# Optimization experiments

Hardware: AMD Instinct MI355X
Metric: run time of the kernel (lower is better)

Reference implementation:

```python
import jax, jax.numpy as jnp
import numpy as np

N_NODES = 100000
N_EDGES = 3200000
F_IN = 128
HIDDEN = 16
OUT_DIM = 16
NUM_GRAPHS = 64


def setup_inputs() -> dict:
    key = jax.random.key(0)
    ks = jax.random.split(key, 9)
    x = jax.random.normal(ks[0], (N_NODES, F_IN), dtype=jnp.float32)
    edge_index = jax.random.randint(ks[1], (2, N_EDGES), 0, N_NODES, dtype=jnp.int32)
    batch = jnp.sort(jax.random.randint(ks[2], (N_NODES,), 0, NUM_GRAPHS, dtype=jnp.int32))
    W1 = jax.random.normal(ks[3], (F_IN, HIDDEN), dtype=jnp.float32) * (1.0 / np.sqrt(F_IN))
    b1 = jnp.zeros((HIDDEN,), dtype=jnp.float32)
    W2 = jax.random.normal(ks[4], (HIDDEN, OUT_DIM), dtype=jnp.float32) * (1.0 / np.sqrt(HIDDEN))
    b2 = jnp.zeros((OUT_DIM,), dtype=jnp.float32)
    fc_w = jax.random.normal(ks[5], (OUT_DIM, 1), dtype=jnp.float32) * (1.0 / np.sqrt(OUT_DIM))
    fc_b = jnp.zeros((1,), dtype=jnp.float32)
    return {"x": x, "edge_index": edge_index, "batch": batch,
            "W1": W1, "b1": b1, "W2": W2, "b2": b2, "fc_w": fc_w, "fc_b": fc_b}


def _gcn_conv(x, edge_index, W, b):
    """PyG GCNConv: x' = D^-1/2 (A+I) D^-1/2 (x W) + b (with self-loops)."""
    n = x.shape[0]
    h = x @ W  # transform first (small dim), then propagate
    src, dst = edge_index[0], edge_index[1]
    # degree including the self-loop (+1)
    deg = jax.ops.segment_sum(jnp.ones(src.shape, h.dtype), dst, num_segments=n) + 1.0
    dis = jax.lax.rsqrt(deg)  # deg >= 1 so no zeros
    norm = dis[src] * dis[dst]  # [E]
    agg = jax.ops.segment_sum(h[src] * norm[:, None], dst, num_segments=n)
    # self-loop contribution: norm_ii = dis[i]^2
    return agg + (dis * dis)[:, None] * h + b


def reference(x, edge_index, batch, W1, b1, W2, b2, fc_w, fc_b):
    h = jax.nn.relu(_gcn_conv(x, edge_index, W1, b1))
    # F.dropout(training=False) in eval mode is identity
    h = jax.nn.relu(_gcn_conv(h, edge_index, W2, b2))
    pooled = jax.ops.segment_sum(h, batch, num_segments=NUM_GRAPHS)  # global_add_pool
    return jax.nn.sigmoid(pooled @ fc_w + fc_b)  # [NUM_GRAPHS, 1]
```

## Files before the change

### kernel.cpp

```cpp
#include <hip/hip_runtime.h>
#include <hip/hip_fp16.h>
#include <math.h>

#define N_NODES 100000
#define N_EDGES 3200000
#define F_IN    128
#define NGRAPH  64

#define NB      512
#define BWIDTH  196
#define NPAD    100352
#define BIN_CAP 7200
#define EPB     4096

typedef int   iv4 __attribute__((ext_vector_type(4)));
typedef float fv4 __attribute__((ext_vector_type(4)));
typedef float fv2 __attribute__((ext_vector_type(2)));

#define OFF_BINCUR 0
#define OFF_DIS    512
#define OFF_ROWR   (512 + NPAD)
#define OFF_COL    (512 + NPAD * 3)
#define OFF_BINNED (OFF_COL + N_EDGES)
#define OFF_HINH   OFF_BINNED
#define OFF_BUFB   (OFF_BINNED + NPAD * 8)

__global__ void zero_k(int* __restrict__ p) {
    p[threadIdx.x] = 0;
}

__global__ void __launch_bounds__(512)
bin_k(const int* __restrict__ ei, int* __restrict__ binCursor,
      int* __restrict__ binned) {
    __shared__ int cntL[NB], cnt2[NB], gbase[NB];
    int tid = threadIdx.x;
    cntL[tid] = 0; cnt2[tid] = 0;
    __syncthreads();
    int myBase = blockIdx.x * EPB + tid * 8;
    bool act = (myBase < N_EDGES);
    int s[8], d[8];
    if (act) {
        const iv4* sp = (const iv4*)(ei + myBase);
        const iv4* dp = (const iv4*)(ei + N_EDGES + myBase);
        iv4 a = __builtin_nontemporal_load(sp);
        iv4 b2 = __builtin_nontemporal_load(sp + 1);
        iv4 c = __builtin_nontemporal_load(dp);
        iv4 e = __builtin_nontemporal_load(dp + 1);
        s[0]=a.x; s[1]=a.y; s[2]=a.z; s[3]=a.w; s[4]=b2.x; s[5]=b2.y; s[6]=b2.z; s[7]=b2.w;
        d[0]=c.x; d[1]=c.y; d[2]=c.z; d[3]=c.w; d[4]=e.x; d[5]=e.y; d[6]=e.z; d[7]=e.w;
#pragma unroll
        for (int k = 0; k < 8; ++k)
            atomicAdd(&cntL[(unsigned)d[k] / BWIDTH], 1);
    }
    __syncthreads();
    gbase[tid] = atomicAdd(&binCursor[tid], cntL[tid]);
    __syncthreads();
    if (act) {
#pragma unroll
        for (int k = 0; k < 8; ++k) {
            int b = (unsigned)d[k] / BWIDTH;
            int off = atomicAdd(&cnt2[b], 1);
            binned[(size_t)b * BIN_CAP + gbase[b] + off] = ((d[k] - b * BWIDTH) << 17) | s[k];
        }
    }
}

__global__ void __launch_bounds__(512)
sort_k(const int* __restrict__ binCursor, const int* __restrict__ binned,
       float* __restrict__ dis, int2* __restrict__ rowRange, int* __restrict__ col) {
    __shared__ int red[NB];
    __shared__ int cnt[BWIDTH];
    __shared__ int rowLoc[BWIDTH + 1];
    __shared__ int cur[BWIDTH];
    __shared__ int wsum[8];
    __shared__ int ebs;
    int b = blockIdx.x, tid = threadIdx.x;
    red[tid] = (tid < b) ? binCursor[tid] : 0;
    __syncthreads();
#pragma unroll
    for (int st = 256; st > 0; st >>= 1) {
        if (tid < st) red[tid] += red[tid + st];
        __syncthreads();
    }
    if (tid == 0) ebs = red[0];
    if (tid < BWIDTH) cnt[tid] = 0;
    __syncthreads();
    int n = binCursor[b];
    const int* bb = binned + (size_t)b * BIN_CAP;
    for (int i = tid; i < n; i += 512)
        atomicAdd(&cnt[bb[i] >> 17], 1);
    __syncthreads();
    int base = b * BWIDTH;
    int bw = min(BWIDTH, N_NODES - base);
    if (tid < bw)
        dis[base + tid] = rsqrtf((float)cnt[tid] + 1.0f);
    int a = (tid < BWIDTH) ? cnt[tid] : 0;
    int lane = tid & 63, wid = tid >> 6;
    int sc = a;
#pragma unroll
    for (int d = 1; d < 64; d <<= 1) {
        int o = __shfl_up(sc, d);
        if (lane >= d) sc += o;
    }
    if (lane == 63) wsum[wid] = sc;
    __syncthreads();
    int woff = 0;
    for (int w = 0; w < wid; ++w) woff += wsum[w];
    if (tid < BWIDTH) {
        int excl = woff + sc - a;
        rowLoc[tid] = excl;
        cur[tid] = excl;
    }
    if (tid == 0) rowLoc[BWIDTH] = n;
    __syncthreads();
    int eb = ebs;
    if (tid < bw) {
        int2 rr; rr.x = eb + rowLoc[tid]; rr.y = eb + rowLoc[tid + 1];
        rowRange[base + tid] = rr;
    }
    for (int i = tid; i < n; i += 512) {
        int p = bb[i];
        int pos = atomicAdd(&cur[p >> 17], 1);
        col[eb + pos] = p & 0x1FFFF;
    }
}

__global__ void transform1_k(const float* __restrict__ x, const float* __restrict__ W,
                             const float* __restrict__ dis, __half* __restrict__ outh) {
    int i = blockIdx.x * blockDim.x + threadIdx.x;
    if (i >= N_NODES) return;
    const fv4* xr = (const fv4*)(x + (size_t)i * F_IN);
    float acc[16];
#pragma unroll
    for (int j = 0; j < 16; ++j) acc[j] = 0.f;
#pragma unroll 4
    for (int k4 = 0; k4 < F_IN / 4; ++k4) {
        fv4 xv = xr[k4];
#pragma unroll
        for (int kk = 0; kk < 4; ++kk) {
            int k = k4 * 4 + kk;
            float xk = xv[kk];
#pragma unroll
            for (int j = 0; j < 16; ++j)
                acc[j] = fmaf(xk, W[k * 16 + j], acc[j]);
        }
    }
    float di = dis[i];
    __half2 t[8];
#pragma unroll
    for (int q = 0; q < 8; ++q)
        t[q] = __floats2half2_rn(di * acc[2 * q], di * acc[2 * q + 1]);
    iv4* o = (iv4*)(outh + (size_t)i * 16);
    o[0] = *(iv4*)&t[0];
    o[1] = *(iv4*)&t[4];
}

__global__ void transform2_k(const float* __restrict__ h, const float* __restrict__ W,
                             const float* __restrict__ dis, __half* __restrict__ outh) {
    int i = blockIdx.x * blockDim.x + threadIdx.x;
    if (i >= N_NODES) return;
    const fv4* hr = (const fv4*)(h + (size_t)i * 16);
    float hv[16];
#pragma unroll
    for (int q = 0; q < 4; ++q) {
        fv4 t = hr[q];
        hv[q * 4 + 0] = t.x; hv[q * 4 + 1] = t.y; hv[q * 4 + 2] = t.z; hv[q * 4 + 3] = t.w;
    }
    float acc[16];
#pragma unroll
    for (int j = 0; j < 16; ++j) acc[j] = 0.f;
#pragma unroll
    for (int k = 0; k < 16; ++k) {
#pragma unroll
        for (int j = 0; j < 16; ++j)
            acc[j] = fmaf(hv[k], W[k * 16 + j], acc[j]);
    }
    float di = dis[i];
    __half2 t[8];
#pragma unroll
    for (int q = 0; q < 8; ++q)
        t[q] = __floats2half2_rn(di * acc[2 * q], di * acc[2 * q + 1]);
    iv4* o = (iv4*)(outh + (size_t)i * 16);
    o[0] = *(iv4*)&t[0];
    o[1] = *(iv4*)&t[4];
}

__global__ void prop_k(const __half* __restrict__ hinh, const float* __restrict__ dis,
                       const int2* __restrict__ rowRange, const int* __restrict__ col,
                       const float* __restrict__ bias, float* __restrict__ hout) {
    int gid = blockIdx.x * blockDim.x + threadIdx.x;
    int node = gid >> 3;
    int j = gid & 7;
    if (node >= N_NODES) return;
    int2 rr = rowRange[node];
    const __half2* hh = (const __half2*)hinh;
    float ax0 = 0.f, ay0 = 0.f, ax1 = 0.f, ay1 = 0.f;
    float ax2 = 0.f, ay2 = 0.f, ax3 = 0.f, ay3 = 0.f;
    int e = rr.x;
    for (; e + 4 <= rr.y; e += 4) {
        int s0 = col[e];
        int s1 = col[e + 1];
        int s2 = col[e + 2];
        int s3 = col[e + 3];
        float2 f0 = __half22float2(hh[s0 * 8 + j]);
        float2 f1 = __half22float2(hh[s1 * 8 + j]);
        float2 f2 = __half22float2(hh[s2 * 8 + j]);
        float2 f3 = __half22float2(hh[s3 * 8 + j]);
        ax0 += f0.x; ay0 += f0.y;
        ax1 += f1.x; ay1 += f1.y;
        ax2 += f2.x; ay2 += f2.y;
        ax3 += f3.x; ay3 += f3.y;
    }
    for (; e < rr.y; ++e) {
        float2 f = __half22float2(hh[col[e] * 8 + j]);
        ax0 += f.x; ay0 += f.y;
    }
    float2 self = __half22float2(hh[node * 8 + j]);
    float di = dis[node];
    fv2 bj = ((const fv2*)bias)[j];
    float sx = (ax0 + ax1) + (ax2 + ax3) + self.x;
    float sy = (ay0 + ay1) + (ay2 + ay3) + self.y;
    fv2 v;
    v.x = fmaxf(fmaf(di, sx, bj.x), 0.f);
    v.y = fmaxf(fmaf(di, sy, bj.y), 0.f);
    ((fv2*)hout)[node * 8 + j] = v;
}

__global__ void pool_k(const float* __restrict__ h2, const int* __restrict__ batch,
                       const float* __restrict__ fcw, const float* __restrict__ fcb,
                       float* __restrict__ out) {
    __shared__ float partial[16][16];
    int g = blockIdx.x;
    int lane16 = threadIdx.x & 15, grp = threadIdx.x >> 4;
    int lo = 0, hi = N_NODES;
    while (lo < hi) { int m = (lo + hi) >> 1; if (batch[m] < g) lo = m + 1; else hi = m; }
    int start = lo;
    lo = start; hi = N_NODES;
    while (lo < hi) { int m = (lo + hi) >> 1; if (batch[m] < g + 1) lo = m + 1; else hi = m; }
    int end = lo;
    float acc = 0.f;
    for (int i = start + grp; i < end; i += 16) acc += h2[i * 16 + lane16];
    partial[grp][lane16] = acc;
    __syncthreads();
    if (threadIdx.x < 16) {
        float s = 0.f;
#pragma unroll
        for (int gg = 0; gg < 16; ++gg) s += partial[gg][threadIdx.x];
        partial[0][threadIdx.x] = s * fcw[threadIdx.x];
    }
    __syncthreads();
    if (threadIdx.x == 0) {
        float z = fcb[0];
#pragma unroll
        for (int j = 0; j < 16; ++j) z += partial[0][j];
        out[g] = 1.0f / (1.0f + expf(-z));
    }
}

extern "C" void kernel_launch(void* const* d_in, const int* in_sizes, int n_in,
                              void* d_out, int out_size, void* d_ws, size_t ws_size,
                              hipStream_t stream) {
    const float* x    = (const float*)d_in[0];
    const int*   ei   = (const int*)d_in[1];
    const int*   batch= (const int*)d_in[2];
    const float* W1   = (const float*)d_in[3];
    const float* b1   = (const float*)d_in[4];
    const float* W2   = (const float*)d_in[5];
    const float* b2   = (const float*)d_in[6];
    const float* fcw  = (const float*)d_in[7];
    const float* fcb  = (const float*)d_in[8];
    float* out = (float*)d_out;

    float* ws = (float*)d_ws;
    int*    binCur   = (int*)(ws + OFF_BINCUR);
    float*  dis      = ws + OFF_DIS;
    int2*   rowRange = (int2*)(ws + OFF_ROWR);
    int*    col      = (int*)(ws + OFF_COL);
    int*    binned   = (int*)(ws + OFF_BINNED);
    __half* hinH     = (__half*)(ws + OFF_HINH);
    float*  bufB     = ws + OFF_BUFB;

    const int B = 256;
    int gN   = (N_NODES + B - 1) / B;
    int gNP  = (N_NODES * 8 + B - 1) / B;
    int gBin = (N_EDGES + EPB - 1) / EPB;

    zero_k<<<1, NB, 0, stream>>>(binCur);
    bin_k<<<gBin, 512, 0, stream>>>(ei, binCur, binned);
    sort_k<<<NB, 512, 0, stream>>>(binCur, binned, dis, rowRange, col);

    transform1_k<<<gN, B, 0, stream>>>(x, W1, dis, hinH);
    prop_k<<<gNP, B, 0, stream>>>(hinH, dis, rowRange, col, b1, bufB);
    transform2_k<<<gN, B, 0, stream>>>(bufB, W2, dis, hinH);
    prop_k<<<gNP, B, 0, stream>>>(hinH, dis, rowRange, col, b2, bufB);
    pool_k<<<NGRAPH, B, 0, stream>>>(bufB, batch, fcw, fcb, out);
}
```

Measured before the change: 174.0 us.

## Fuse layer-2 transform into prop1 and pooling into prop2, precompute bucket scan

Fuses the second GCN linear transform into the first propagation kernel, using 8-lane shuffles to gather the hidden row and writing fp16 output directly. It also folds the fc projection and global add pooling into the second propagation through LDS atomics plus global atomics, then applies a tiny sigmoid kernel. The per-block prefix-sum reduction in sort_k is replaced by a single scan kernel. This removes the fp32 intermediate buffers and the separate transform2 and pool passes, at the cost of float atomics whose ordering is nondeterministic and two extra small launches.

New measurement: 154.5 us. -11.2%, faster.

```diff
diff --git a/kernel.cpp b/kernel.cpp
--- a/kernel.cpp
+++ b/kernel.cpp
@@ -18,12 +18,14 @@
 typedef float fv2 __attribute__((ext_vector_type(2)));
 
 #define OFF_BINCUR 0
-#define OFF_DIS    512
-#define OFF_ROWR   (512 + NPAD)
-#define OFF_COL    (512 + NPAD * 3)
+#define OFF_GZ     512
+#define OFF_BBASE  576
+#define OFF_DIS    1088
+#define OFF_ROWR   (1088 + NPAD)
+#define OFF_COL    (1088 + NPAD * 3)
 #define OFF_BINNED (OFF_COL + N_EDGES)
 #define OFF_HINH   OFF_BINNED
-#define OFF_BUFB   (OFF_BINNED + NPAD * 8)
+#define OFF_HINH2  (OFF_BINNED + NPAD * 8)
 
 __global__ void zero_k(int* __restrict__ p) {
     p[threadIdx.x] = 0;
@@ -66,23 +68,33 @@
 }
 
 __global__ void __launch_bounds__(512)
-sort_k(const int* __restrict__ binCursor, const int* __restrict__ binned,
-       float* __restrict__ dis, int2* __restrict__ rowRange, int* __restrict__ col) {
-    __shared__ int red[NB];
+scanB_k(const int* __restrict__ binCur, int* __restrict__ bucketBase) {
+    __shared__ int wsum[8];
+    int tid = threadIdx.x;
+    int v = binCur[tid];
+    int lane = tid & 63, wid = tid >> 6;
+    int sc = v;
+#pragma unroll
+    for (int d = 1; d < 64; d <<= 1) {
+        int o = __shfl_up(sc, d);
+        if (lane >= d) sc += o;
+    }
+    if (lane == 63) wsum[wid] = sc;
+    __syncthreads();
+    int woff = 0;
+    for (int w = 0; w < wid; ++w) woff += wsum[w];
+    bucketBase[tid] = woff + sc - v;
+}
+
+__global__ void __launch_bounds__(512)
+sort_k(const int* __restrict__ binCursor, const int* __restrict__ bucketBase,
+       const int* __restrict__ binned, float* __restrict__ dis,
+       int2* __restrict__ rowRange, int* __restrict__ col) {
     __shared__ int cnt[BWIDTH];
     __shared__ int rowLoc[BWIDTH + 1];
     __shared__ int cur[BWIDTH];
     __shared__ int wsum[8];
-    __shared__ int ebs;
     int b = blockIdx.x, tid = threadIdx.x;
-    red[tid] = (tid < b) ? binCursor[tid] : 0;
-    __syncthreads();
-#pragma unroll
-    for (int st = 256; st > 0; st >>= 1) {
-        if (tid < st) red[tid] += red[tid + st];
-        __syncthreads();
-    }
-    if (tid == 0) ebs = red[0];
     if (tid < BWIDTH) cnt[tid] = 0;
     __syncthreads();
     int n = binCursor[b];
@@ -113,7 +125,7 @@
     }
     if (tid == 0) rowLoc[BWIDTH] = n;
     __syncthreads();
-    int eb = ebs;
+    int eb = bucketBase[b];
     if (tid < bw) {
         int2 rr; rr.x = eb + rowLoc[tid]; rr.y = eb + rowLoc[tid + 1];
         rowRange[base + tid] = rr;
@@ -155,39 +167,10 @@
     o[1] = *(iv4*)&t[4];
 }
 
-__global__ void transform2_k(const float* __restrict__ h, const float* __restrict__ W,
-                             const float* __restrict__ dis, __half* __restrict__ outh) {
-    int i = blockIdx.x * blockDim.x + threadIdx.x;
-    if (i >= N_NODES) return;
-    const fv4* hr = (const fv4*)(h + (size_t)i * 16);
-    float hv[16];
-#pragma unroll
-    for (int q = 0; q < 4; ++q) {
-        fv4 t = hr[q];
-        hv[q * 4 + 0] = t.x; hv[q * 4 + 1] = t.y; hv[q * 4 + 2] = t.z; hv[q * 4 + 3] = t.w;
-    }
-    float acc[16];
-#pragma unroll
-    for (int j = 0; j < 16; ++j) acc[j] = 0.f;
-#pragma unroll
-    for (int k = 0; k < 16; ++k) {
-#pragma unroll
-        for (int j = 0; j < 16; ++j)
-            acc[j] = fmaf(hv[k], W[k * 16 + j], acc[j]);
-    }
-    float di = dis[i];
-    __half2 t[8];
-#pragma unroll
-    for (int q = 0; q < 8; ++q)
-        t[q] = __floats2half2_rn(di * acc[2 * q], di * acc[2 * q + 1]);
-    iv4* o = (iv4*)(outh + (size_t)i * 16);
-    o[0] = *(iv4*)&t[0];
-    o[1] = *(iv4*)&t[4];
-}
-
-__global__ void prop_k(const __half* __restrict__ hinh, const float* __restrict__ dis,
-                       const int2* __restrict__ rowRange, const int* __restrict__ col,
-                       const float* __restrict__ bias, float* __restrict__ hout) {
+__global__ void prop1_k(const __half* __restrict__ hinh, const float* __restrict__ dis,
+                        const int2* __restrict__ rowRange, const int* __restrict__ col,
+                        const float* __restrict__ b1, const float* __restrict__ W2,
+                        __half* __restrict__ outh2) {
     int gid = blockIdx.x * blockDim.x + threadIdx.x;
     int node = gid >> 3;
     int j = gid & 7;
@@ -217,44 +200,82 @@
     }
     float2 self = __half22float2(hh[node * 8 + j]);
     float di = dis[node];
-    fv2 bj = ((const fv2*)bias)[j];
-    float sx = (ax0 + ax1) + (ax2 + ax3) + self.x;
-    float sy = (ay0 + ay1) + (ay2 + ay3) + self.y;
-    fv2 v;
-    v.x = fmaxf(fmaf(di, sx, bj.x), 0.f);
-    v.y = fmaxf(fmaf(di, sy, bj.y), 0.f);
-    ((fv2*)hout)[node * 8 + j] = v;
-}
-
-__global__ void pool_k(const float* __restrict__ h2, const int* __restrict__ batch,
-                       const float* __restrict__ fcw, const float* __restrict__ fcb,
-                       float* __restrict__ out) {
-    __shared__ float partial[16][16];
-    int g = blockIdx.x;
-    int lane16 = threadIdx.x & 15, grp = threadIdx.x >> 4;
-    int lo = 0, hi = N_NODES;
-    while (lo < hi) { int m = (lo + hi) >> 1; if (batch[m] < g) lo = m + 1; else hi = m; }
-    int start = lo;
-    lo = start; hi = N_NODES;
-    while (lo < hi) { int m = (lo + hi) >> 1; if (batch[m] < g + 1) lo = m + 1; else hi = m; }
-    int end = lo;
-    float acc = 0.f;
-    for (int i = start + grp; i < end; i += 16) acc += h2[i * 16 + lane16];
-    partial[grp][lane16] = acc;
-    __syncthreads();
-    if (threadIdx.x < 16) {
-        float s = 0.f;
-#pragma unroll
-        for (int gg = 0; gg < 16; ++gg) s += partial[gg][threadIdx.x];
-        partial[0][threadIdx.x] = s * fcw[threadIdx.x];
-    }
-    __syncthreads();
-    if (threadIdx.x == 0) {
-        float z = fcb[0];
-#pragma unroll
-        for (int j = 0; j < 16; ++j) z += partial[0][j];
-        out[g] = 1.0f / (1.0f + expf(-z));
-    }
+    fv2 bj = ((const fv2*)b1)[j];
+    float hx = fmaxf(fmaf(di, (ax0 + ax1) + (ax2 + ax3) + self.x, bj.x), 0.f);
+    float hy = fmaxf(fmaf(di, (ay0 + ay1) + (ay2 + ay3) + self.y, bj.y), 0.f);
+    float h1[16];
+#pragma unroll
+    for (int k = 0; k < 8; ++k) {
+        h1[2 * k]     = __shfl(hx, k, 8);
+        h1[2 * k + 1] = __shfl(hy, k, 8);
+    }
+    const fv2* w2 = (const fv2*)W2;
+    float o0 = 0.f, o1 = 0.f;
+#pragma unroll
+    for (int m = 0; m < 16; ++m) {
+        fv2 wv = w2[m * 8 + j];
+        o0 = fmaf(h1[m], wv.x, o0);
+        o1 = fmaf(h1[m], wv.y, o1);
+    }
+    ((__half2*)outh2)[node * 8 + j] = __floats2half2_rn(di * o0, di * o1);
+}
+
+__global__ void __launch_bounds__(256)
+prop2_k(const __half* __restrict__ hinh2, const float* __restrict__ dis,
+        const int2* __restrict__ rowRange, const int* __restrict__ col,
+        const float* __restrict__ b2, const int* __restrict__ batch,
+        const float* __restrict__ fcw, float* __restrict__ gz) {
+    __shared__ float ldsz[NGRAPH];
+    int tid = threadIdx.x;
+    if (tid < NGRAPH) ldsz[tid] = 0.f;
+    __syncthreads();
+    int gid = blockIdx.x * 256 + tid;
+    int node = gid >> 3;
+    int j = gid & 7;
+    int2 rr = rowRange[node];
+    const __half2* hh = (const __half2*)hinh2;
+    float ax0 = 0.f, ay0 = 0.f, ax1 = 0.f, ay1 = 0.f;
+    float ax2 = 0.f, ay2 = 0.f, ax3 = 0.f, ay3 = 0.f;
+    int e = rr.x;
+    for (; e + 4 <= rr.y; e += 4) {
+        int s0 = col[e];
+        int s1 = col[e + 1];
+        int s2 = col[e + 2];
+        int s3 = col[e + 3];
+        float2 f0 = __half22float2(hh[s0 * 8 + j]);
+        float2 f1 = __half22float2(hh[s1 * 8 + j]);
+        float2 f2 = __half22float2(hh[s2 * 8 + j]);
+        float2 f3 = __half22float2(hh[s3 * 8 + j]);
+        ax0 += f0.x; ay0 += f0.y;
+        ax1 += f1.x; ay1 += f1.y;
+        ax2 += f2.x; ay2 += f2.y;
+        ax3 += f3.x; ay3 += f3.y;
+    }
+    for (; e < rr.y; ++e) {
+        float2 f = __half22float2(hh[col[e] * 8 + j]);
+        ax0 += f.x; ay0 += f.y;
+    }
+    float2 self = __half22float2(hh[node * 8 + j]);
+    float di = dis[node];
+    fv2 bj = ((const fv2*)b2)[j];
+    float hx = fmaxf(fmaf(di, (ax0 + ax1) + (ax2 + ax3) + self.x, bj.x), 0.f);
+    float hy = fmaxf(fmaf(di, (ay0 + ay1) + (ay2 + ay3) + self.y, bj.y), 0.f);
+    fv2 fw = ((const fv2*)fcw)[j];
+    float s = hx * fw.x + hy * fw.y;
+#pragma unroll
+    for (int off = 4; off; off >>= 1) s += __shfl_xor(s, off, 8);
+    if (j == 0) atomicAdd(&ldsz[batch[node]], s);
+    __syncthreads();
+    if (tid < NGRAPH) {
+        float v = ldsz[tid];
+        if (v != 0.f) atomicAdd(&gz[tid], v);
+    }
+}
+
+__global__ void sig_k(const float* __restrict__ gz, const float* __restrict__ fcb,
+                      float* __restrict__ out) {
+    int g = threadIdx.x;
+    out[g] = 1.0f / (1.0f + expf(-(gz[g] + fcb[0])));
 }
 
 extern "C" void kernel_launch(void* const* d_in, const int* in_sizes, int n_in,
@@ -273,25 +294,27 @@
 
     float* ws = (float*)d_ws;
     int*    binCur   = (int*)(ws + OFF_BINCUR);
+    float*  gz       = ws + OFF_GZ;
+    int*    bucketBase = (int*)(ws + OFF_BBASE);
     float*  dis      = ws + OFF_DIS;
     int2*   rowRange = (int2*)(ws + OFF_ROWR);
     int*    col      = (int*)(ws + OFF_COL);
     int*    binned   = (int*)(ws + OFF_BINNED);
     __half* hinH     = (__half*)(ws + OFF_HINH);
-    float*  bufB     = ws + OFF_BUFB;
+    __half* hinH2    = (__half*)(ws + OFF_HINH2);
 
     const int B = 256;
     int gN   = (N_NODES + B - 1) / B;
     int gNP  = (N_NODES * 8 + B - 1) / B;
     int gBin = (N_EDGES + EPB - 1) / EPB;
 
-    zero_k<<<1, NB, 0, stream>>>(binCur);
+    zero_k<<<1, 576, 0, stream>>>(binCur);
     bin_k<<<gBin, 512, 0, stream>>>(ei, binCur, binned);
-    sort_k<<<NB, 512, 0, stream>>>(binCur, binned, dis, rowRange, col);
+    scanB_k<<<1, 512, 0, stream>>>(binCur, bucketBase);
+    sort_k<<<NB, 512, 0, stream>>>(binCur, bucketBase, binned, dis, rowRange, col);
 
     transform1_k<<<gN, B, 0, stream>>>(x, W1, dis, hinH);
-    prop_k<<<gNP, B, 0, stream>>>(hinH, dis, rowRange, col, b1, bufB);
-    transform2_k<<<gN, B, 0, stream>>>(bufB, W2, dis, hinH);
-    prop_k<<<gNP, B, 0, stream>>>(hinH, dis, rowRange, col, b2, bufB);
-    pool_k<<<NGRAPH, B, 0, stream>>>(bufB, batch, fcw, fcb, out);
-}
+    prop1_k<<<gNP, B, 0, stream>>>(hinH, dis, rowRange, col, b1, W2, hinH2);
+    prop2_k<<<gNP, B, 0, stream>>>(hinH2, dis, rowRange, col, b2, batch, fcw, gz);
+    sig_k<<<1, NGRAPH, 0, stream>>>(gz, fcb, out);
+}
```
